# Kernel optimization log

Hardware: AMD Instinct MI355X
Metric: run time of the kernel (lower is better)

Reference implementation:

```python
import jax, jax.numpy as jnp
import numpy as np

MARGIN = 1.0
EPS = 1e-10


def setup_inputs() -> dict:
    key = jax.random.key(0)
    k1, k2, k3 = jax.random.split(key, 3)
    C, D = 4096, 1024
    B, A = 8, 32
    cls_features = jax.random.normal(k1, (C, D), dtype=jnp.float32)
    prototypes = jax.random.normal(k2, (C, D), dtype=jnp.float32)
    annotations = jax.random.randint(k3, (B, A, 5), 0, C, dtype=jnp.int64)
    return {"cls_features": cls_features, "prototypes": prototypes,
            "annotations": annotations, "steps": 1000}


def reference(cls_features, prototypes, annotations, steps):
    C, D = cls_features.shape
    protos = jax.lax.stop_gradient(prototypes)  # prototypes.detach()

    # one_hot presence of each class in the batch annotations (col 4 = class id, -1 = pad)
    targets = annotations[:, :, 4]                      # [B, A]
    valid = targets != -1
    counts = jnp.zeros((C,), jnp.float32).at[
        jnp.where(valid, targets, 0).ravel()
    ].add(valid.astype(jnp.float32).ravel())
    mask_i = counts > 0                                  # class present in batch
    mask_j = jnp.sum(protos, axis=-1) != 0               # prototypes[j].sum() != 0

    # pairwise mean squared distance: msd[i, j] = mean((feat_i - proto_j)^2)
    f2 = jnp.sum(cls_features * cls_features, axis=-1)   # [C]
    p2 = jnp.sum(protos * protos, axis=-1)               # [C]
    cross = cls_features @ protos.T                      # [C, C]
    msd = jnp.maximum(f2[:, None] + p2[None, :] - 2.0 * cross, 0.0) / D

    pair_mask = mask_i[:, None] & mask_j[None, :]
    eye = jnp.eye(C, dtype=bool)
    intra_mask = pair_mask & eye
    inter_mask = pair_mask & ~eye

    intra_count = jnp.sum(intra_mask.astype(jnp.float32))
    inter_count = jnp.sum(inter_mask.astype(jnp.float32))

    intra_loss = jnp.sum(jnp.where(intra_mask, msd, 0.0)) / (intra_count + EPS)

    s = jnp.sqrt(jnp.maximum(msd, 1e-12))
    e = MARGIN - s
    inter_term = (e / MARGIN) ** 2 * jnp.maximum(e, 0.0) ** 2
    inter_loss = jnp.sum(jnp.where(inter_mask, inter_term, 0.0)) / (inter_count + EPS)

    return (intra_loss, inter_loss)
```

## Files before the change

kernel.cpp:

```cpp
#include <hip/hip_runtime.h>
#include <hip/hip_bf16.h>

typedef float f32x4 __attribute__((ext_vector_type(4)));
typedef int   i32x4 __attribute__((ext_vector_type(4)));
typedef int   i32x8 __attribute__((ext_vector_type(8)));

#define NC 4096
#define ND 1024
#define NVP 256
#define EPSF 1e-10f
#define SCALE1 127


__global__ __launch_bounds__(256)
void fprep_kernel(const int* __restrict__ ann, int n_ann,
                  const float* __restrict__ F,
                  unsigned char* __restrict__ Fc, float* __restrict__ f2c,
                  int* __restrict__ vidx, int* __restrict__ nv,
                  float* __restrict__ accum) {
  __shared__ unsigned char mark[NC];
  __shared__ int wsum[4];
  __shared__ int vloc[NVP];
  __shared__ float rs[4];
  const int tid = threadIdx.x;
  const int lane = tid & 63, wid = tid >> 6;

  for (int i = tid; i < NC; i += 256) mark[i] = 0;
  __syncthreads();
  for (int t = tid; t < n_ann; t += 256) {
    int idx = ann[t * 5 + 4];
    if (idx >= 0 && idx < NC) mark[idx] = 1;
  }
  __syncthreads();
  int base = tid * 16, lc = 0;
  #pragma unroll
  for (int k = 0; k < 16; ++k) lc += mark[base + k];
  int inc = lc;
  #pragma unroll
  for (int off = 1; off < 64; off <<= 1) {
    int v = __shfl_up(inc, off);
    if (lane >= off) inc += v;
  }
  if (lane == 63) wsum[wid] = inc;
  __syncthreads();
  int wbase = 0;
  for (int w = 0; w < wid; ++w) wbase += wsum[w];
  int pos = wbase + inc - lc;
  for (int k = 0; k < 16; ++k)
    if (mark[base + k]) vloc[pos++] = base + k;
  const int total = wsum[0] + wsum[1] + wsum[2] + wsum[3];
  __syncthreads();

  if (blockIdx.x == 0) {
    for (int i = tid; i < NVP; i += 256) vidx[i] = (i < total) ? vloc[i] : 0;
    if (tid == 0) *nv = total;
    if (tid < 8) accum[tid] = 0.f;
  }

  const int slot = blockIdx.x;
  if (slot >= total) return;

  const int row = vloc[slot];
  float4 v = *reinterpret_cast<const float4*>(F + (size_t)row * ND + tid * 4);
  int pk = __builtin_amdgcn_cvt_pk_fp8_f32(v.x, v.y, 0, false);
  pk = __builtin_amdgcn_cvt_pk_fp8_f32(v.z, v.w, pk, true);
  {
    int d0 = tid * 4;
    int kt = d0 >> 7, hif = (d0 >> 5) & 3, half = (d0 >> 4) & 1, b = d0 & 15;
    int R16 = slot >> 4, lof = slot & 15;
    size_t fa = ((((size_t)kt * 16 + R16) * 2 + half) * 64 + hif * 16 + lof) * 16 + b;
    *reinterpret_cast<int*>(Fc + fa) = pk;
  }
  float sq = v.x * v.x + v.y * v.y + v.z * v.z + v.w * v.w;
  #pragma unroll
  for (int off = 32; off; off >>= 1) sq += __shfl_down(sq, off);
  if (lane == 0) rs[wid] = sq;
  __syncthreads();
  if (tid == 0) f2c[slot] = rs[0] + rs[1] + rs[2] + rs[3];
}

#define LDFRAG(V, BASEPTR, FID)                                               \
  do {                                                                        \
    const unsigned char* _p = (BASEPTR) + (size_t)(FID) * 2048 + lane * 16;   \
    i32x4 _l0 = *(const i32x4*)(_p);                                          \
    i32x4 _l1 = *(const i32x4*)(_p + 1024);                                   \
    V = __builtin_shufflevector(_l0, _l1, 0, 1, 2, 3, 4, 5, 6, 7);            \
  } while (0)

__global__ __launch_bounds__(512)
void pgemm_kernel(const float* __restrict__ P,
                  const unsigned char* __restrict__ Fc,
                  const float* __restrict__ f2c,
                  const int* __restrict__ vidx, const int* __restrict__ nv,
                  float* __restrict__ psum, float* __restrict__ accum) {
  __shared__ __attribute__((aligned(16))) unsigned char bfrag[8 * 2048];
  __shared__ float p2l[16], psl[16], redI[8], redE[8];
  const int tid = threadIdx.x;
  const int lane = tid & 63, wid = tid >> 6;
  const int bj = blockIdx.x;

  {
    const int r = tid >> 5;
    const int seg = tid & 31;
    const float* src = P + (size_t)(bj * 16 + r) * ND;
    float sq = 0.f, sm = 0.f;
    #pragma unroll
    for (int i = 0; i < 8; ++i) {
      float4 v = *reinterpret_cast<const float4*>(src + (seg + i * 32) * 4);
      int pk = __builtin_amdgcn_cvt_pk_fp8_f32(v.x, v.y, 0, false);
      pk = __builtin_amdgcn_cvt_pk_fp8_f32(v.z, v.w, pk, true);
      int addr = i * 2048 + r * 128 + ((seg * 4) ^ ((r & 7) << 4));
      *reinterpret_cast<int*>(&bfrag[addr]) = pk;
      sq += v.x * v.x + v.y * v.y + v.z * v.z + v.w * v.w;
      sm += v.x + v.y + v.z + v.w;
    }
    #pragma unroll
    for (int off = 16; off; off >>= 1) {
      sq += __shfl_down(sq, off, 32);
      sm += __shfl_down(sm, off, 32);
    }
    if ((tid & 31) == 0) {
      p2l[r] = sq; psl[r] = sm;
      psum[bj * 16 + r] = sm;
    }
  }
  __syncthreads();

  const int lo = lane & 15, hi = lane >> 4;
  f32x4 acc0 = {0.f, 0.f, 0.f, 0.f}, acc1 = acc0;
  const int fbase = wid * 2;
  #pragma unroll 4
  for (int kt = 0; kt < 8; ++kt) {
    i32x8 a0, a1, b;
    LDFRAG(a0, Fc, kt * 16 + fbase);
    LDFRAG(a1, Fc, kt * 16 + fbase + 1);
    {
      int x = (lo & 7) << 4;
      const unsigned char* bb = &bfrag[kt * 2048 + lo * 128];
      i32x4 l0 = *reinterpret_cast<const i32x4*>(bb + ((hi * 32) ^ x));
      i32x4 l1 = *reinterpret_cast<const i32x4*>(bb + ((hi * 32 + 16) ^ x));
      b = __builtin_shufflevector(l0, l1, 0, 1, 2, 3, 4, 5, 6, 7);
    }
    acc0 = __builtin_amdgcn_mfma_scale_f32_16x16x128_f8f6f4(
        a0, b, acc0, 0, 0, 0, SCALE1, 0, SCALE1);
    acc1 = __builtin_amdgcn_mfma_scale_f32_16x16x128_f8f6f4(
        a1, b, acc1, 0, 0, 0, SCALE1, 0, SCALE1);
  }

  int Nv = *nv;
  float intra_l = 0.f, inter_l = 0.f;
  const int gj = bj * 16 + lo;
  const float p2j = p2l[lo];
  const bool mj = psl[lo] != 0.f;
  if (mj) {
    #pragma unroll
    for (int f = 0; f < 2; ++f) {
      f32x4 a = f ? acc1 : acc0;
      #pragma unroll
      for (int r = 0; r < 4; ++r) {
        int ci = wid * 32 + f * 16 + hi * 4 + r;
        if (ci < Nv) {
          float msd = fmaxf(f2c[ci] + p2j - 2.f * a[r], 0.f) * (1.f / 1024.f);
          int gi = vidx[ci];
          if (gi == gj) {
            intra_l += msd;
          } else if (msd < 1.0f) {
            float s = sqrtf(fmaxf(msd, 1e-12f));
            float e = 1.f - s;
            float e2 = e * e;
            inter_l += e2 * e2;
          }
        }
      }
    }
  }
  #pragma unroll
  for (int off = 32; off; off >>= 1) {
    intra_l += __shfl_down(intra_l, off);
    inter_l += __shfl_down(inter_l, off);
  }
  if (lane == 0) { redI[wid] = intra_l; redE[wid] = inter_l; }
  __syncthreads();
  if (tid == 0) {
    float si = 0.f, se = 0.f;
    #pragma unroll
    for (int w = 0; w < 8; ++w) { si += redI[w]; se += redE[w]; }
    atomicAdd(&accum[0], si);
    atomicAdd(&accum[1], se);
  }
}

__global__ void finalize_kernel(const float* __restrict__ psum,
                                const int* __restrict__ vidx,
                                const int* __restrict__ nv,
                                const float* __restrict__ accum,
                                float* __restrict__ out) {
  __shared__ int r1[4], r2[4];
  int tid = threadIdx.x;
  int Nv = *nv;
  int nj = 0, nd = 0;
  for (int i = tid; i < NC; i += 256) nj += (psum[i] != 0.f);
  for (int c = tid; c < Nv; c += 256) nd += (psum[vidx[c]] != 0.f);
  #pragma unroll
  for (int off = 32; off; off >>= 1) {
    nj += __shfl_down(nj, off);
    nd += __shfl_down(nd, off);
  }
  int wid = tid >> 6, lane = tid & 63;
  if (lane == 0) { r1[wid] = nj; r2[wid] = nd; }
  __syncthreads();
  if (tid == 0) {
    float fni = (float)Nv;
    float fnj = (float)(r1[0] + r1[1] + r1[2] + r1[3]);
    float fnd = (float)(r2[0] + r2[1] + r2[2] + r2[3]);
    out[0] = accum[0] / (fnd + EPSF);
    out[1] = accum[1] / (fni * fnj - fnd + EPSF);
  }
}

extern "C" void kernel_launch(void* const* d_in, const int* in_sizes, int n_in,
                              void* d_out, int out_size, void* d_ws, size_t ws_size,
                              hipStream_t stream) {
  const float* F = (const float*)d_in[0];
  const float* P = (const float*)d_in[1];
  const int* ann = (const int*)d_in[2];
  int n_ann = in_sizes[2] / 5;

  char* ws = (char*)d_ws;
  unsigned char* Fc = (unsigned char*)ws;
  float* f2c   = (float*)(ws + (size_t)NVP * ND);
  float* psum  = f2c + NVP;
  float* accum = psum + NC;
  int*   vidx  = (int*)(accum + 8);
  int*   nv    = vidx + NVP;

  float* out = (float*)d_out;

  fprep_kernel<<<NVP, 256, 0, stream>>>(ann, n_ann, F, Fc, f2c, vidx, nv, accum);
  pgemm_kernel<<<NC / 16, 512, 0, stream>>>(P, Fc, f2c, vidx, nv, psum, accum);
  finalize_kernel<<<1, 256, 0, stream>>>(psum, vidx, nv, accum, out);
}
```

Before: 28.56 us.

## Fuse prep, GEMM and finalize into one cooperative kernel with grid syncs

Merges the three launches into a single cooperative kernel of 256 blocks that uses grid.sync() between the feature-prep phase, the FP8 MFMA distance phase and the final reduction. Every block recomputes the valid-class list in shared memory, so the index arrays no longer go through global memory. This removes two kernel launch gaps, at the cost of cooperative-launch overhead, two grid-wide barriers, and redundant per-block scanning of the annotations.

```diff
diff --git a/kernel.cpp b/kernel.cpp
--- a/kernel.cpp
+++ b/kernel.cpp
@@ -1,5 +1,8 @@
 #include <hip/hip_runtime.h>
+#include <hip/hip_cooperative_groups.h>
 #include <hip/hip_bf16.h>
+
+namespace cg = cooperative_groups;
 
 typedef float f32x4 __attribute__((ext_vector_type(4)));
 typedef int   i32x4 __attribute__((ext_vector_type(4)));
@@ -11,73 +14,6 @@
 #define EPSF 1e-10f
 #define SCALE1 127
 
-
-__global__ __launch_bounds__(256)
-void fprep_kernel(const int* __restrict__ ann, int n_ann,
-                  const float* __restrict__ F,
-                  unsigned char* __restrict__ Fc, float* __restrict__ f2c,
-                  int* __restrict__ vidx, int* __restrict__ nv,
-                  float* __restrict__ accum) {
-  __shared__ unsigned char mark[NC];
-  __shared__ int wsum[4];
-  __shared__ int vloc[NVP];
-  __shared__ float rs[4];
-  const int tid = threadIdx.x;
-  const int lane = tid & 63, wid = tid >> 6;
-
-  for (int i = tid; i < NC; i += 256) mark[i] = 0;
-  __syncthreads();
-  for (int t = tid; t < n_ann; t += 256) {
-    int idx = ann[t * 5 + 4];
-    if (idx >= 0 && idx < NC) mark[idx] = 1;
-  }
-  __syncthreads();
-  int base = tid * 16, lc = 0;
-  #pragma unroll
-  for (int k = 0; k < 16; ++k) lc += mark[base + k];
-  int inc = lc;
-  #pragma unroll
-  for (int off = 1; off < 64; off <<= 1) {
-    int v = __shfl_up(inc, off);
-    if (lane >= off) inc += v;
-  }
-  if (lane == 63) wsum[wid] = inc;
-  __syncthreads();
-  int wbase = 0;
-  for (int w = 0; w < wid; ++w) wbase += wsum[w];
-  int pos = wbase + inc - lc;
-  for (int k = 0; k < 16; ++k)
-    if (mark[base + k]) vloc[pos++] = base + k;
-  const int total = wsum[0] + wsum[1] + wsum[2] + wsum[3];
-  __syncthreads();
-
-  if (blockIdx.x == 0) {
-    for (int i = tid; i < NVP; i += 256) vidx[i] = (i < total) ? vloc[i] : 0;
-    if (tid == 0) *nv = total;
-    if (tid < 8) accum[tid] = 0.f;
-  }
-
-  const int slot = blockIdx.x;
-  if (slot >= total) return;
-
-  const int row = vloc[slot];
-  float4 v = *reinterpret_cast<const float4*>(F + (size_t)row * ND + tid * 4);
-  int pk = __builtin_amdgcn_cvt_pk_fp8_f32(v.x, v.y, 0, false);
-  pk = __builtin_amdgcn_cvt_pk_fp8_f32(v.z, v.w, pk, true);
-  {
-    int d0 = tid * 4;
-    int kt = d0 >> 7, hif = (d0 >> 5) & 3, half = (d0 >> 4) & 1, b = d0 & 15;
-    int R16 = slot >> 4, lof = slot & 15;
-    size_t fa = ((((size_t)kt * 16 + R16) * 2 + half) * 64 + hif * 16 + lof) * 16 + b;
-    *reinterpret_cast<int*>(Fc + fa) = pk;
-  }
-  float sq = v.x * v.x + v.y * v.y + v.z * v.z + v.w * v.w;
-  #pragma unroll
-  for (int off = 32; off; off >>= 1) sq += __shfl_down(sq, off);
-  if (lane == 0) rs[wid] = sq;
-  __syncthreads();
-  if (tid == 0) f2c[slot] = rs[0] + rs[1] + rs[2] + rs[3];
-}
 
 #define LDFRAG(V, BASEPTR, FID)                                               \
   do {                                                                        \
@@ -87,22 +23,86 @@
     V = __builtin_shufflevector(_l0, _l1, 0, 1, 2, 3, 4, 5, 6, 7);            \
   } while (0)
 
-__global__ __launch_bounds__(512)
-void pgemm_kernel(const float* __restrict__ P,
-                  const unsigned char* __restrict__ Fc,
-                  const float* __restrict__ f2c,
-                  const int* __restrict__ vidx, const int* __restrict__ nv,
-                  float* __restrict__ psum, float* __restrict__ accum) {
+__global__ __launch_bounds__(512, 1)
+void fused_kernel(const int* __restrict__ ann, int n_ann,
+                  const float* __restrict__ F, const float* __restrict__ P,
+                  unsigned char* __restrict__ Fc, float* __restrict__ f2c,
+                  float* __restrict__ psum, float* __restrict__ accum,
+                  float* __restrict__ out) {
+  cg::grid_group grid = cg::this_grid();
+  __shared__ unsigned char mark[NC];
+  __shared__ int vloc[NVP];
+  __shared__ int wsum[8];
+  __shared__ float rs[8];
   __shared__ __attribute__((aligned(16))) unsigned char bfrag[8 * 2048];
   __shared__ float p2l[16], psl[16], redI[8], redE[8];
+  __shared__ int fin1[8], fin2[8];
+
   const int tid = threadIdx.x;
   const int lane = tid & 63, wid = tid >> 6;
-  const int bj = blockIdx.x;
+  const int bid = blockIdx.x;
+
+  for (int i = tid; i < NC; i += 512) mark[i] = 0;
+  __syncthreads();
+  for (int t = tid; t < n_ann; t += 512) {
+    int idx = ann[t * 5 + 4];
+    if (idx >= 0 && idx < NC) mark[idx] = 1;
+  }
+  __syncthreads();
+  int lc = 0;
+  {
+    int base = tid * 8;
+    #pragma unroll
+    for (int k = 0; k < 8; ++k) lc += mark[base + k];
+  }
+  int inc = lc;
+  #pragma unroll
+  for (int off = 1; off < 64; off <<= 1) {
+    int v = __shfl_up(inc, off);
+    if (lane >= off) inc += v;
+  }
+  if (lane == 63) wsum[wid] = inc;
+  __syncthreads();
+  int wbase = 0;
+  for (int w = 0; w < wid; ++w) wbase += wsum[w];
+  int pos = wbase + inc - lc;
+  {
+    int base = tid * 8;
+    for (int k = 0; k < 8; ++k)
+      if (mark[base + k]) vloc[pos++] = base + k;
+  }
+  const int total = wsum[0] + wsum[1] + wsum[2] + wsum[3] +
+                    wsum[4] + wsum[5] + wsum[6] + wsum[7];
+  __syncthreads();
+  for (int i = total + tid; i < NVP; i += 512) vloc[i] = 0;
+  if (bid == 0 && tid < 8) accum[tid] = 0.f;
+  __syncthreads();
+
+  if (bid < total) {
+    if (tid < 256) {
+      const int row = vloc[bid];
+      float4 v = *reinterpret_cast<const float4*>(F + (size_t)row * ND + tid * 4);
+      int pk = __builtin_amdgcn_cvt_pk_fp8_f32(v.x, v.y, 0, false);
+      pk = __builtin_amdgcn_cvt_pk_fp8_f32(v.z, v.w, pk, true);
+      int d0 = tid * 4;
+      int kt = d0 >> 7, hif = (d0 >> 5) & 3, half = (d0 >> 4) & 1, b = d0 & 15;
+      int R16 = bid >> 4, lof = bid & 15;
+      size_t fa = ((((size_t)kt * 16 + R16) * 2 + half) * 64 + hif * 16 + lof) * 16 + b;
+      *reinterpret_cast<int*>(Fc + fa) = pk;
+      float sq = v.x * v.x + v.y * v.y + v.z * v.z + v.w * v.w;
+      #pragma unroll
+      for (int off = 32; off; off >>= 1) sq += __shfl_down(sq, off);
+      if (lane == 0) rs[wid] = sq;
+    }
+    __syncthreads();
+    if (tid == 0) f2c[bid] = rs[0] + rs[1] + rs[2] + rs[3];
+  }
+  grid.sync();
 
   {
     const int r = tid >> 5;
     const int seg = tid & 31;
-    const float* src = P + (size_t)(bj * 16 + r) * ND;
+    const float* src = P + (size_t)(bid * 16 + r) * ND;
     float sq = 0.f, sm = 0.f;
     #pragma unroll
     for (int i = 0; i < 8; ++i) {
@@ -121,7 +121,7 @@
     }
     if ((tid & 31) == 0) {
       p2l[r] = sq; psl[r] = sm;
-      psum[bj * 16 + r] = sm;
+      psum[bid * 16 + r] = sm;
     }
   }
   __syncthreads();
@@ -147,28 +147,29 @@
         a1, b, acc1, 0, 0, 0, SCALE1, 0, SCALE1);
   }
 
-  int Nv = *nv;
   float intra_l = 0.f, inter_l = 0.f;
-  const int gj = bj * 16 + lo;
-  const float p2j = p2l[lo];
-  const bool mj = psl[lo] != 0.f;
-  if (mj) {
-    #pragma unroll
-    for (int f = 0; f < 2; ++f) {
-      f32x4 a = f ? acc1 : acc0;
+  {
+    const int gj = bid * 16 + lo;
+    const float p2j = p2l[lo];
+    const bool mj = psl[lo] != 0.f;
+    if (mj) {
       #pragma unroll
-      for (int r = 0; r < 4; ++r) {
-        int ci = wid * 32 + f * 16 + hi * 4 + r;
-        if (ci < Nv) {
-          float msd = fmaxf(f2c[ci] + p2j - 2.f * a[r], 0.f) * (1.f / 1024.f);
-          int gi = vidx[ci];
-          if (gi == gj) {
-            intra_l += msd;
-          } else if (msd < 1.0f) {
-            float s = sqrtf(fmaxf(msd, 1e-12f));
-            float e = 1.f - s;
-            float e2 = e * e;
-            inter_l += e2 * e2;
+      for (int f = 0; f < 2; ++f) {
+        f32x4 a = f ? acc1 : acc0;
+        #pragma unroll
+        for (int r = 0; r < 4; ++r) {
+          int ci = wid * 32 + f * 16 + hi * 4 + r;
+          if (ci < total) {
+            float msd = fmaxf(f2c[ci] + p2j - 2.f * a[r], 0.f) * (1.f / 1024.f);
+            int gi = vloc[ci];
+            if (gi == gj) {
+              intra_l += msd;
+            } else if (msd < 1.0f) {
+              float s = sqrtf(fmaxf(msd, 1e-12f));
+              float e = 1.f - s;
+              float e2 = e * e;
+              inter_l += e2 * e2;
+            }
           }
         }
       }
@@ -188,42 +189,36 @@
     atomicAdd(&accum[0], si);
     atomicAdd(&accum[1], se);
   }
-}
-
-__global__ void finalize_kernel(const float* __restrict__ psum,
-                                const int* __restrict__ vidx,
-                                const int* __restrict__ nv,
-                                const float* __restrict__ accum,
-                                float* __restrict__ out) {
-  __shared__ int r1[4], r2[4];
-  int tid = threadIdx.x;
-  int Nv = *nv;
-  int nj = 0, nd = 0;
-  for (int i = tid; i < NC; i += 256) nj += (psum[i] != 0.f);
-  for (int c = tid; c < Nv; c += 256) nd += (psum[vidx[c]] != 0.f);
-  #pragma unroll
-  for (int off = 32; off; off >>= 1) {
-    nj += __shfl_down(nj, off);
-    nd += __shfl_down(nd, off);
-  }
-  int wid = tid >> 6, lane = tid & 63;
-  if (lane == 0) { r1[wid] = nj; r2[wid] = nd; }
-  __syncthreads();
-  if (tid == 0) {
-    float fni = (float)Nv;
-    float fnj = (float)(r1[0] + r1[1] + r1[2] + r1[3]);
-    float fnd = (float)(r2[0] + r2[1] + r2[2] + r2[3]);
-    out[0] = accum[0] / (fnd + EPSF);
-    out[1] = accum[1] / (fni * fnj - fnd + EPSF);
+  grid.sync();
+
+  if (bid == 0) {
+    int nj = 0, nd = 0;
+    for (int i = tid; i < NC; i += 512) nj += (psum[i] != 0.f);
+    for (int c = tid; c < total; c += 512) nd += (psum[vloc[c]] != 0.f);
+    #pragma unroll
+    for (int off = 32; off; off >>= 1) {
+      nj += __shfl_down(nj, off);
+      nd += __shfl_down(nd, off);
+    }
+    if (lane == 0) { fin1[wid] = nj; fin2[wid] = nd; }
+    __syncthreads();
+    if (tid == 0) {
+      float fnj = 0.f, fnd = 0.f;
+      #pragma unroll
+      for (int w = 0; w < 8; ++w) { fnj += fin1[w]; fnd += fin2[w]; }
+      float fni = (float)total;
+      out[0] = accum[0] / (fnd + EPSF);
+      out[1] = accum[1] / (fni * fnj - fnd + EPSF);
+    }
   }
 }
 
 extern "C" void kernel_launch(void* const* d_in, const int* in_sizes, int n_in,
                               void* d_out, int out_size, void* d_ws, size_t ws_size,
                               hipStream_t stream) {
+  const int* ann = (const int*)d_in[2];
   const float* F = (const float*)d_in[0];
   const float* P = (const float*)d_in[1];
-  const int* ann = (const int*)d_in[2];
   int n_ann = in_sizes[2] / 5;
 
   char* ws = (char*)d_ws;
@@ -231,12 +226,11 @@
   float* f2c   = (float*)(ws + (size_t)NVP * ND);
   float* psum  = f2c + NVP;
   float* accum = psum + NC;
-  int*   vidx  = (int*)(accum + 8);
-  int*   nv    = vidx + NVP;
-
   float* out = (float*)d_out;
 
-  fprep_kernel<<<NVP, 256, 0, stream>>>(ann, n_ann, F, Fc, f2c, vidx, nv, accum);
-  pgemm_kernel<<<NC / 16, 512, 0, stream>>>(P, Fc, f2c, vidx, nv, psum, accum);
-  finalize_kernel<<<1, 256, 0, stream>>>(psum, vidx, nv, accum, out);
+  void* args[] = {(void*)&ann, (void*)&n_ann, (void*)&F, (void*)&P,
+                  (void*)&Fc, (void*)&f2c, (void*)&psum, (void*)&accum,
+                  (void*)&out};
+  hipLaunchCooperativeKernel((const void*)fused_kernel, dim3(NC / 16),
+                             dim3(512), args, 0, stream);
 }
```

New measurement: 84.39 us. 2.95x slower.

## Split prototype FP8 conversion into separate kernel and precompute fragment layout

Applied to the files above, without the earlier changes.

Moves the prototype fp32-to-fp8 conversion and its norm/sum reductions out of the GEMM kernel into a dedicated pconv kernel. That kernel spreads the work over 8x more blocks and writes prototypes straight into the MFMA fragment layout in global memory. The mask compaction becomes a single-block kernel, and the feature conversion becomes its own kernel that reads the compacted indices. The GEMM kernel then loads B fragments directly from global memory instead of staging through LDS. The trade-off is two extra kernel launches, a full fp8 copy of the prototypes round-tripped through memory, and atomics for the row reductions.

```diff
diff --git a/kernel.cpp b/kernel.cpp
--- a/kernel.cpp
+++ b/kernel.cpp
@@ -13,19 +13,15 @@
 
 
 __global__ __launch_bounds__(256)
-void fprep_kernel(const int* __restrict__ ann, int n_ann,
-                  const float* __restrict__ F,
-                  unsigned char* __restrict__ Fc, float* __restrict__ f2c,
-                  int* __restrict__ vidx, int* __restrict__ nv,
-                  float* __restrict__ accum) {
+void mask_compact_kernel(const int* __restrict__ ann, int n_ann,
+                         int* __restrict__ vidx, int* __restrict__ nv,
+                         float* __restrict__ accum,
+                         float* __restrict__ p2, float* __restrict__ psum) {
   __shared__ unsigned char mark[NC];
   __shared__ int wsum[4];
-  __shared__ int vloc[NVP];
-  __shared__ float rs[4];
   const int tid = threadIdx.x;
   const int lane = tid & 63, wid = tid >> 6;
-
-  for (int i = tid; i < NC; i += 256) mark[i] = 0;
+  for (int i = tid; i < NC; i += 256) { mark[i] = 0; p2[i] = 0.f; psum[i] = 0.f; }
   __syncthreads();
   for (int t = tid; t < n_ann; t += 256) {
     int idx = ann[t * 5 + 4];
@@ -47,20 +43,23 @@
   for (int w = 0; w < wid; ++w) wbase += wsum[w];
   int pos = wbase + inc - lc;
   for (int k = 0; k < 16; ++k)
-    if (mark[base + k]) vloc[pos++] = base + k;
+    if (mark[base + k]) vidx[pos++] = base + k;
   const int total = wsum[0] + wsum[1] + wsum[2] + wsum[3];
-  __syncthreads();
-
-  if (blockIdx.x == 0) {
-    for (int i = tid; i < NVP; i += 256) vidx[i] = (i < total) ? vloc[i] : 0;
-    if (tid == 0) *nv = total;
-    if (tid < 8) accum[tid] = 0.f;
-  }
-
+  if (tid == 0) *nv = total;
+  for (int i = total + tid; i < NVP; i += 256) vidx[i] = 0;
+  if (tid < 8) accum[tid] = 0.f;
+}
+
+__global__ __launch_bounds__(256)
+void fconv_kernel(const float* __restrict__ F, const int* __restrict__ vidx,
+                  const int* __restrict__ nv, unsigned char* __restrict__ Fc,
+                  float* __restrict__ f2c) {
+  __shared__ float rs[4];
   const int slot = blockIdx.x;
-  if (slot >= total) return;
-
-  const int row = vloc[slot];
+  const int tid = threadIdx.x;
+  const int lane = tid & 63, wid = tid >> 6;
+  if (slot >= *nv) return;
+  const int row = vidx[slot];
   float4 v = *reinterpret_cast<const float4*>(F + (size_t)row * ND + tid * 4);
   int pk = __builtin_amdgcn_cvt_pk_fp8_f32(v.x, v.y, 0, false);
   pk = __builtin_amdgcn_cvt_pk_fp8_f32(v.z, v.w, pk, true);
@@ -79,6 +78,45 @@
   if (tid == 0) f2c[slot] = rs[0] + rs[1] + rs[2] + rs[3];
 }
 
+__global__ __launch_bounds__(256)
+void pconv_kernel(const float* __restrict__ P, unsigned char* __restrict__ Pc,
+                  float* __restrict__ p2, float* __restrict__ psum) {
+  __shared__ __attribute__((aligned(8))) unsigned char lbuf[16 * 128];
+  const int g = blockIdx.x >> 3;
+  const int kt = blockIdx.x & 7;
+  const int tid = threadIdx.x;
+  const int r = tid >> 4;
+  const int c = tid & 15;
+  const float* src = P + (size_t)(g * 16 + r) * ND + kt * 128 + c * 8;
+  float4 va = *reinterpret_cast<const float4*>(src);
+  float4 vb = *reinterpret_cast<const float4*>(src + 4);
+  int i0 = __builtin_amdgcn_cvt_pk_fp8_f32(va.x, va.y, 0, false);
+  i0 = __builtin_amdgcn_cvt_pk_fp8_f32(va.z, va.w, i0, true);
+  int i1 = __builtin_amdgcn_cvt_pk_fp8_f32(vb.x, vb.y, 0, false);
+  i1 = __builtin_amdgcn_cvt_pk_fp8_f32(vb.z, vb.w, i1, true);
+  *reinterpret_cast<int*>(&lbuf[r * 128 + c * 8]) = i0;
+  *reinterpret_cast<int*>(&lbuf[r * 128 + c * 8 + 4]) = i1;
+  float sq = va.x * va.x + va.y * va.y + va.z * va.z + va.w * va.w +
+             vb.x * vb.x + vb.y * vb.y + vb.z * vb.z + vb.w * vb.w;
+  float sm = va.x + va.y + va.z + va.w + vb.x + vb.y + vb.z + vb.w;
+  #pragma unroll
+  for (int off = 8; off; off >>= 1) {
+    sq += __shfl_down(sq, off, 16);
+    sm += __shfl_down(sm, off, 16);
+  }
+  if (c == 0) {
+    atomicAdd(&p2[g * 16 + r], sq);
+    atomicAdd(&psum[g * 16 + r], sm);
+  }
+  __syncthreads();
+  const int o = tid * 8;
+  const int half = o >> 10, lanef = (o & 1023) >> 4, b0 = o & 15;
+  const int lo = lanef & 15, hi = lanef >> 4;
+  unsigned long long val =
+      *reinterpret_cast<const unsigned long long*>(&lbuf[lo * 128 + hi * 32 + half * 16 + b0]);
+  *reinterpret_cast<unsigned long long*>(Pc + (size_t)(kt * 256 + g) * 2048 + o) = val;
+}
+
 #define LDFRAG(V, BASEPTR, FID)                                               \
   do {                                                                        \
     const unsigned char* _p = (BASEPTR) + (size_t)(FID) * 2048 + lane * 16;   \
@@ -88,44 +126,15 @@
   } while (0)
 
 __global__ __launch_bounds__(512)
-void pgemm_kernel(const float* __restrict__ P,
-                  const unsigned char* __restrict__ Fc,
-                  const float* __restrict__ f2c,
-                  const int* __restrict__ vidx, const int* __restrict__ nv,
-                  float* __restrict__ psum, float* __restrict__ accum) {
-  __shared__ __attribute__((aligned(16))) unsigned char bfrag[8 * 2048];
-  __shared__ float p2l[16], psl[16], redI[8], redE[8];
+void gemm_loss_kernel(const unsigned char* __restrict__ Fc,
+                      const unsigned char* __restrict__ Pc,
+                      const float* __restrict__ f2c, const float* __restrict__ p2,
+                      const float* __restrict__ psum, const int* __restrict__ vidx,
+                      const int* __restrict__ nv, float* __restrict__ accum) {
+  __shared__ float redI[8], redE[8];
+  const int bj = blockIdx.x;
   const int tid = threadIdx.x;
   const int lane = tid & 63, wid = tid >> 6;
-  const int bj = blockIdx.x;
-
-  {
-    const int r = tid >> 5;
-    const int seg = tid & 31;
-    const float* src = P + (size_t)(bj * 16 + r) * ND;
-    float sq = 0.f, sm = 0.f;
-    #pragma unroll
-    for (int i = 0; i < 8; ++i) {
-      float4 v = *reinterpret_cast<const float4*>(src + (seg + i * 32) * 4);
-      int pk = __builtin_amdgcn_cvt_pk_fp8_f32(v.x, v.y, 0, false);
-      pk = __builtin_amdgcn_cvt_pk_fp8_f32(v.z, v.w, pk, true);
-      int addr = i * 2048 + r * 128 + ((seg * 4) ^ ((r & 7) << 4));
-      *reinterpret_cast<int*>(&bfrag[addr]) = pk;
-      sq += v.x * v.x + v.y * v.y + v.z * v.z + v.w * v.w;
-      sm += v.x + v.y + v.z + v.w;
-    }
-    #pragma unroll
-    for (int off = 16; off; off >>= 1) {
-      sq += __shfl_down(sq, off, 32);
-      sm += __shfl_down(sm, off, 32);
-    }
-    if ((tid & 31) == 0) {
-      p2l[r] = sq; psl[r] = sm;
-      psum[bj * 16 + r] = sm;
-    }
-  }
-  __syncthreads();
-
   const int lo = lane & 15, hi = lane >> 4;
   f32x4 acc0 = {0.f, 0.f, 0.f, 0.f}, acc1 = acc0;
   const int fbase = wid * 2;
@@ -134,24 +143,17 @@
     i32x8 a0, a1, b;
     LDFRAG(a0, Fc, kt * 16 + fbase);
     LDFRAG(a1, Fc, kt * 16 + fbase + 1);
-    {
-      int x = (lo & 7) << 4;
-      const unsigned char* bb = &bfrag[kt * 2048 + lo * 128];
-      i32x4 l0 = *reinterpret_cast<const i32x4*>(bb + ((hi * 32) ^ x));
-      i32x4 l1 = *reinterpret_cast<const i32x4*>(bb + ((hi * 32 + 16) ^ x));
-      b = __builtin_shufflevector(l0, l1, 0, 1, 2, 3, 4, 5, 6, 7);
-    }
+    LDFRAG(b, Pc, kt * 256 + bj);
     acc0 = __builtin_amdgcn_mfma_scale_f32_16x16x128_f8f6f4(
         a0, b, acc0, 0, 0, 0, SCALE1, 0, SCALE1);
     acc1 = __builtin_amdgcn_mfma_scale_f32_16x16x128_f8f6f4(
         a1, b, acc1, 0, 0, 0, SCALE1, 0, SCALE1);
   }
-
-  int Nv = *nv;
+  const int total = *nv;
   float intra_l = 0.f, inter_l = 0.f;
   const int gj = bj * 16 + lo;
-  const float p2j = p2l[lo];
-  const bool mj = psl[lo] != 0.f;
+  const float p2j = p2[gj];
+  const bool mj = psum[gj] != 0.f;
   if (mj) {
     #pragma unroll
     for (int f = 0; f < 2; ++f) {
@@ -159,7 +161,7 @@
       #pragma unroll
       for (int r = 0; r < 4; ++r) {
         int ci = wid * 32 + f * 16 + hi * 4 + r;
-        if (ci < Nv) {
+        if (ci < total) {
           float msd = fmaxf(f2c[ci] + p2j - 2.f * a[r], 0.f) * (1.f / 1024.f);
           int gi = vidx[ci];
           if (gi == gj) {
@@ -227,16 +229,20 @@
   int n_ann = in_sizes[2] / 5;
 
   char* ws = (char*)d_ws;
-  unsigned char* Fc = (unsigned char*)ws;
-  float* f2c   = (float*)(ws + (size_t)NVP * ND);
-  float* psum  = f2c + NVP;
+  unsigned char* Pc = (unsigned char*)ws;
+  unsigned char* Fc = (unsigned char*)(ws + (size_t)NC * ND);
+  float* f2c   = (float*)(ws + (size_t)NC * ND + (size_t)NVP * ND);
+  float* p2    = f2c + NVP;
+  float* psum  = p2 + NC;
   float* accum = psum + NC;
   int*   vidx  = (int*)(accum + 8);
   int*   nv    = vidx + NVP;
 
   float* out = (float*)d_out;
 
-  fprep_kernel<<<NVP, 256, 0, stream>>>(ann, n_ann, F, Fc, f2c, vidx, nv, accum);
-  pgemm_kernel<<<NC / 16, 512, 0, stream>>>(P, Fc, f2c, vidx, nv, psum, accum);
+  mask_compact_kernel<<<1, 256, 0, stream>>>(ann, n_ann, vidx, nv, accum, p2, psum);
+  fconv_kernel<<<NVP, 256, 0, stream>>>(F, vidx, nv, Fc, f2c);
+  pconv_kernel<<<NC / 16 * 8, 256, 0, stream>>>(P, Pc, p2, psum);
+  gemm_loss_kernel<<<NC / 16, 512, 0, stream>>>(Fc, Pc, f2c, p2, psum, vidx, nv, accum);
   finalize_kernel<<<1, 256, 0, stream>>>(psum, vidx, nv, accum, out);
 }
```

Measured after the change: 34.19 us. 19.7% more time.

## Split class compaction into zero, atomic-compact, and convert kernels

Applied to the files above, without the earlier changes.

Replaces the per-block redundant mark/prefix-scan compaction (every one of 256 blocks rebuilt the valid-class list) with a single-block atomic compaction kernel preceded by a zeroing kernel, then a conversion kernel reads the shared list. This removes the duplicated scan work in each block but adds two extra kernel launches and serial dependencies. The atomic ordering makes vidx order nondeterministic, which does not change the sums but may alter float summation order slightly.

```diff
diff --git a/kernel.cpp b/kernel.cpp
--- a/kernel.cpp
+++ b/kernel.cpp
@@ -12,55 +12,40 @@
 #define SCALE1 127
 
 
+__global__ void zero_kernel(int* __restrict__ seen, float* __restrict__ accum,
+                            int* __restrict__ nv) {
+  int i = blockIdx.x * 256 + threadIdx.x;
+  if (i < NC) seen[i] = 0;
+  if (i < 8) accum[i] = 0.f;
+  if (i == 8) *nv = 0;
+}
+
+__global__ void compact_kernel(const int* __restrict__ ann, int n_ann,
+                               int* __restrict__ seen, int* __restrict__ vidx,
+                               int* __restrict__ nv) {
+  int t = threadIdx.x;
+  for (; t < n_ann; t += 256) {
+    int idx = ann[t * 5 + 4];
+    if (idx >= 0 && idx < NC) {
+      int old = atomicExch(&seen[idx], 1);
+      if (old == 0) {
+        int slot = atomicAdd(nv, 1);
+        vidx[slot] = idx;
+      }
+    }
+  }
+}
+
 __global__ __launch_bounds__(256)
-void fprep_kernel(const int* __restrict__ ann, int n_ann,
-                  const float* __restrict__ F,
-                  unsigned char* __restrict__ Fc, float* __restrict__ f2c,
-                  int* __restrict__ vidx, int* __restrict__ nv,
-                  float* __restrict__ accum) {
-  __shared__ unsigned char mark[NC];
-  __shared__ int wsum[4];
-  __shared__ int vloc[NVP];
+void fconv_kernel(const float* __restrict__ F, const int* __restrict__ vidx,
+                  const int* __restrict__ nv, unsigned char* __restrict__ Fc,
+                  float* __restrict__ f2c) {
   __shared__ float rs[4];
+  const int slot = blockIdx.x;
   const int tid = threadIdx.x;
   const int lane = tid & 63, wid = tid >> 6;
-
-  for (int i = tid; i < NC; i += 256) mark[i] = 0;
-  __syncthreads();
-  for (int t = tid; t < n_ann; t += 256) {
-    int idx = ann[t * 5 + 4];
-    if (idx >= 0 && idx < NC) mark[idx] = 1;
-  }
-  __syncthreads();
-  int base = tid * 16, lc = 0;
-  #pragma unroll
-  for (int k = 0; k < 16; ++k) lc += mark[base + k];
-  int inc = lc;
-  #pragma unroll
-  for (int off = 1; off < 64; off <<= 1) {
-    int v = __shfl_up(inc, off);
-    if (lane >= off) inc += v;
-  }
-  if (lane == 63) wsum[wid] = inc;
-  __syncthreads();
-  int wbase = 0;
-  for (int w = 0; w < wid; ++w) wbase += wsum[w];
-  int pos = wbase + inc - lc;
-  for (int k = 0; k < 16; ++k)
-    if (mark[base + k]) vloc[pos++] = base + k;
-  const int total = wsum[0] + wsum[1] + wsum[2] + wsum[3];
-  __syncthreads();
-
-  if (blockIdx.x == 0) {
-    for (int i = tid; i < NVP; i += 256) vidx[i] = (i < total) ? vloc[i] : 0;
-    if (tid == 0) *nv = total;
-    if (tid < 8) accum[tid] = 0.f;
-  }
-
-  const int slot = blockIdx.x;
-  if (slot >= total) return;
-
-  const int row = vloc[slot];
+  if (slot >= *nv) return;
+  const int row = vidx[slot];
   float4 v = *reinterpret_cast<const float4*>(F + (size_t)row * ND + tid * 4);
   int pk = __builtin_amdgcn_cvt_pk_fp8_f32(v.x, v.y, 0, false);
   pk = __builtin_amdgcn_cvt_pk_fp8_f32(v.z, v.w, pk, true);
@@ -147,7 +132,7 @@
         a1, b, acc1, 0, 0, 0, SCALE1, 0, SCALE1);
   }
 
-  int Nv = *nv;
+  const int total = *nv;
   float intra_l = 0.f, inter_l = 0.f;
   const int gj = bj * 16 + lo;
   const float p2j = p2l[lo];
@@ -159,7 +144,7 @@
       #pragma unroll
       for (int r = 0; r < 4; ++r) {
         int ci = wid * 32 + f * 16 + hi * 4 + r;
-        if (ci < Nv) {
+        if (ci < total) {
           float msd = fmaxf(f2c[ci] + p2j - 2.f * a[r], 0.f) * (1.f / 1024.f);
           int gi = vidx[ci];
           if (gi == gj) {
@@ -233,10 +218,13 @@
   float* accum = psum + NC;
   int*   vidx  = (int*)(accum + 8);
   int*   nv    = vidx + NVP;
+  int*   seen  = nv + 1;
 
   float* out = (float*)d_out;
 
-  fprep_kernel<<<NVP, 256, 0, stream>>>(ann, n_ann, F, Fc, f2c, vidx, nv, accum);
+  zero_kernel<<<16, 256, 0, stream>>>(seen, accum, nv);
+  compact_kernel<<<1, 256, 0, stream>>>(ann, n_ann, seen, vidx, nv);
+  fconv_kernel<<<NVP, 256, 0, stream>>>(F, vidx, nv, Fc, f2c);
   pgemm_kernel<<<NC / 16, 512, 0, stream>>>(P, Fc, f2c, vidx, nv, psum, accum);
   finalize_kernel<<<1, 256, 0, stream>>>(psum, vidx, nv, accum, out);
 }
```

Measured after the change: 33.54 us. 1.17x slower.
